# Performance work log

Measured on AMD Instinct MI355X. Metric: run time of the kernel, lower is better.

Reference implementation:

```python
import jax, jax.numpy as jnp
import numpy as np

B, L, H, C, A = 8, 4096, 512, 64, 512
NEG = -1000000000.0

def setup_inputs() -> dict:
    key = jax.random.key(0)
    ks = jax.random.split(key, 6)
    hidden_states = jax.random.normal(ks[0], (B, L, H), dtype=jnp.float32)
    critical_mask = jax.random.randint(ks[1], (B, L, 1), 0, 2).astype(bool)
    count_active_channels = jax.random.randint(ks[2], (B, L, 1), 0, 64).astype(jnp.int32)
    channel_activity = jax.random.normal(ks[3], (B, L, C), dtype=jnp.float32)
    proj_w = jax.random.normal(ks[4], (H, A), dtype=jnp.float32) * 0.02
    proj_b = jnp.zeros((A,), dtype=jnp.float32)
    score_w = jax.random.normal(ks[5], (A, 1), dtype=jnp.float32) * 0.02
    score_b = jnp.zeros((1,), dtype=jnp.float32)
    return {"hidden_states": hidden_states, "critical_mask": critical_mask,
            "count_active_channels": count_active_channels,
            "channel_activity": channel_activity,
            "proj_w": proj_w, "proj_b": proj_b,
            "score_w": score_w, "score_b": score_b}

def reference(hidden_states, critical_mask, count_active_channels, channel_activity,
              proj_w, proj_b, score_w, score_b):
    mask = critical_mask[..., 0].astype(bool)                       # (B,L)
    count_signal = count_active_channels[..., 0].astype(hidden_states.dtype)  # (B,L)
    activity = jnp.maximum(channel_activity.astype(hidden_states.dtype), 0.0)  # (B,L,C)
    # score(tanh(proj(h)))  -> (B,L)
    logits = (jnp.tanh(hidden_states @ proj_w + proj_b) @ score_w + score_b)[..., 0]
    logits = logits + jnp.log1p(jnp.maximum(count_signal, 0.0))
    channel_mask = activity > 0                                      # (B,L,C)
    # (B,C,L) masked logits with log1p activity bias
    channel_logits = logits[:, None, :] + jnp.log1p(jnp.swapaxes(activity, 1, 2))
    channel_logits = jnp.where(jnp.swapaxes(channel_mask, 1, 2), channel_logits, NEG)
    has_channel_any = channel_mask.any(axis=1)                       # (B,C)
    weights = jax.nn.softmax(channel_logits, axis=-1)                # (B,C,L)
    weights = jnp.where(has_channel_any[..., None], weights, 0.0)
    channel_contexts = jnp.einsum('bcl,blh->bch', weights, hidden_states)  # (B,C,H)
    fallback = jnp.broadcast_to(hidden_states[:, -1:, :], channel_contexts.shape)
    channel_contexts = jnp.where(has_channel_any[..., None], channel_contexts, fallback)
    mix = activity / jnp.maximum(activity.sum(axis=2, keepdims=True), 1.0)  # (B,L,C)
    expanded_context = jnp.einsum('blc,bch->blh', mix, channel_contexts)    # (B,L,H)
    max_count = jnp.maximum(count_signal.max(axis=1, keepdims=True), 1.0)
    density_gate = 1.0 + count_signal / max_count                    # (B,L)
    attended = jnp.where(mask[..., None], expanded_context * density_gate[..., None], hidden_states)
    return attended, weights
```

## Files before the change

### kernel.cpp

```cpp
#include <hip/hip_runtime.h>
#include <hip/hip_bf16.h>
#include <math.h>

#define NEGV (-1000000000.0f)
constexpr int Bb = 8, Ll = 4096, Hh = 512, Cc = 64, Aa = 512;

typedef float f32x4 __attribute__((ext_vector_type(4)));
typedef short s16x8 __attribute__((ext_vector_type(8)));

__device__ inline ushort f2bf(float f) {
  union { float f; uint u; } v; v.f = f;
  uint u = v.u;
  return (ushort)((u + 0x7FFFu + ((u >> 16) & 1u)) >> 16);
}

__device__ inline uint bfpack2(float x, float y) {
  __hip_bfloat162 h = __float22bfloat162_rn(make_float2(x, y));
  union { __hip_bfloat162 h; uint u; } v; v.h = h;
  return v.u;
}

__global__ void k_init(const int* __restrict__ cnt, const float* __restrict__ sb,
                       float* __restrict__ logits, int* __restrict__ cmax) {
  int i = blockIdx.x * 256 + threadIdx.x;
  int c = cnt[i];
  logits[i] = sb[0] + log1pf(fmaxf((float)c, 0.f));
  int m = c;
#pragma unroll
  for (int s = 32; s; s >>= 1) m = max(m, __shfl_xor(m, s));
  if ((threadIdx.x & 63) == 0) atomicMax(&cmax[i >> 12], m);
}

__global__ void kT_pw(const float* __restrict__ pw, ushort* __restrict__ pwT) {
  __shared__ ushort s[64][65];
  const int k0 = (blockIdx.x >> 3) * 64, a0 = (blockIdx.x & 7) * 64;
  const int t = threadIdx.x;
#pragma unroll
  for (int i = 0; i < 16; ++i) {
    int e = t + i * 256;
    int kk = e >> 6, aa = e & 63;
    s[aa][kk] = f2bf(pw[(size_t)(k0 + kk) * Aa + a0 + aa]);
  }
  __syncthreads();
#pragma unroll
  for (int i = 0; i < 16; ++i) {
    int e = t + i * 256;
    int aa = e >> 6, kk = e & 63;
    pwT[(size_t)(a0 + aa) * Hh + k0 + kk] = s[aa][kk];
  }
}

__global__ __launch_bounds__(256) void k0_gemm(
    const float* __restrict__ hid, const ushort* __restrict__ pwT,
    const float* __restrict__ pb, const float* __restrict__ sw,
    float* __restrict__ logits) {
  __shared__ ushort At[128 * 40];
  __shared__ ushort Bt[128 * 40];
  const int bm = blockIdx.x, bn = blockIdx.y;
  const int tid = threadIdx.x;
  const int lane = tid & 63;
  const int w = tid >> 6;
  const int wm = w >> 1, wn = w & 1;
  const int lc = lane & 15, lq = lane >> 4;

  const int sr = tid >> 1;
  const int sk = (tid & 1) * 16;

  const float* Ag = hid + ((size_t)(bm * 128 + sr)) * Hh + sk;
  const ushort* Bg = pwT + ((size_t)(bn * 128 + sr)) * Hh + sk;

  f32x4 acc[4][4];
#pragma unroll
  for (int mi = 0; mi < 4; ++mi)
#pragma unroll
    for (int ni = 0; ni < 4; ++ni) acc[mi][ni] = (f32x4){0.f, 0.f, 0.f, 0.f};

  int aoff[4], boff[4];
#pragma unroll
  for (int i = 0; i < 4; ++i) {
    aoff[i] = (wm * 64 + i * 16 + lc) * 40 + lq * 8;
    boff[i] = (wn * 64 + i * 16 + lc) * 40 + lq * 8;
  }

  float4 a0 = *(const float4*)(Ag + 0), a1 = *(const float4*)(Ag + 4),
         a2 = *(const float4*)(Ag + 8), a3 = *(const float4*)(Ag + 12);
  uint4 b0 = *(const uint4*)(Bg + 0), b1 = *(const uint4*)(Bg + 8);

  for (int kb = 0; kb < 16; ++kb) {
    __syncthreads();
    uint4 p0 = {bfpack2(a0.x, a0.y), bfpack2(a0.z, a0.w),
                bfpack2(a1.x, a1.y), bfpack2(a1.z, a1.w)};
    uint4 p1 = {bfpack2(a2.x, a2.y), bfpack2(a2.z, a2.w),
                bfpack2(a3.x, a3.y), bfpack2(a3.z, a3.w)};
    *(uint4*)(At + sr * 40 + sk) = p0;
    *(uint4*)(At + sr * 40 + sk + 8) = p1;
    *(uint4*)(Bt + sr * 40 + sk) = b0;
    *(uint4*)(Bt + sr * 40 + sk + 8) = b1;
    __syncthreads();
    if (kb < 15) {
      const float* ag = Ag + (kb + 1) * 32;
      const ushort* bg = Bg + (kb + 1) * 32;
      a0 = *(const float4*)(ag + 0); a1 = *(const float4*)(ag + 4);
      a2 = *(const float4*)(ag + 8); a3 = *(const float4*)(ag + 12);
      b0 = *(const uint4*)(bg + 0); b1 = *(const uint4*)(bg + 8);
    }
    s16x8 af[4], bf[4];
#pragma unroll
    for (int mi = 0; mi < 4; ++mi) af[mi] = *(const s16x8*)(At + aoff[mi]);
#pragma unroll
    for (int ni = 0; ni < 4; ++ni) bf[ni] = *(const s16x8*)(Bt + boff[ni]);
#pragma unroll
    for (int mi = 0; mi < 4; ++mi)
#pragma unroll
      for (int ni = 0; ni < 4; ++ni)
        acc[mi][ni] = __builtin_amdgcn_mfma_f32_16x16x32_bf16(
            af[mi], bf[ni], acc[mi][ni], 0, 0, 0);
  }

  float pbv[4], swv[4];
#pragma unroll
  for (int ni = 0; ni < 4; ++ni) {
    int n = bn * 128 + wn * 64 + ni * 16 + lc;
    pbv[ni] = pb[n];
    swv[ni] = sw[n];
  }
#pragma unroll
  for (int mi = 0; mi < 4; ++mi) {
#pragma unroll
    for (int r = 0; r < 4; ++r) {
      float s = 0.f;
#pragma unroll
      for (int ni = 0; ni < 4; ++ni) {
        float x = acc[mi][ni][r] + pbv[ni];
        float e = __expf(2.f * x);
        float th = 1.f - 2.f / (e + 1.f);
        s = fmaf(th, swv[ni], s);
      }
      s += __shfl_xor(s, 1);
      s += __shfl_xor(s, 2);
      s += __shfl_xor(s, 4);
      s += __shfl_xor(s, 8);
      if (lc == 0) {
        int m = bm * 128 + wm * 64 + mi * 16 + lq * 4 + r;
        atomicAdd(&logits[m], s);
      }
    }
  }
}

__global__ void k2_transpose(const float* __restrict__ act,
                             float* __restrict__ actT,
                             float* __restrict__ dinv) {
  __shared__ float t64[64][65];
  const int b = blockIdx.x >> 6;
  const int l0 = (blockIdx.x & 63) * 64;
  const int tid = threadIdx.x;
#pragma unroll
  for (int i = 0; i < 16; ++i) {
    int e = tid + i * 256;
    int l = e >> 6, c = e & 63;
    float v = act[((size_t)(b * Ll + l0 + l)) * Cc + c];
    t64[l][c] = fmaxf(v, 0.f);
  }
  __syncthreads();
  if (tid < 64) {
    float s = 0.f;
#pragma unroll 8
    for (int c = 0; c < 64; ++c) s += t64[tid][c];
    dinv[b * Ll + l0 + tid] = 1.0f / fmaxf(s, 1.0f);
  }
#pragma unroll
  for (int i = 0; i < 16; ++i) {
    int e = tid + i * 256;
    int c = e >> 6, lq = e & 63;
    actT[((size_t)(b * Cc + c)) * Ll + l0 + lq] = t64[lq][c];
  }
}

__global__ void k3_softmax(const float* __restrict__ actT,
                           const float* __restrict__ logits,
                           float* __restrict__ wout,
                           ushort* __restrict__ wb16,
                           int* __restrict__ hasany) {
  __shared__ float rmax[4], rcnt[4], rsum[4];
  const int bid = blockIdx.x;
  const int b = bid >> 6;
  const int tid = threadIdx.x;
  const float* arow = actT + (size_t)bid * Ll;

  float xs[16];
  float lmax = NEGV, fcnt = 0.f;
#pragma unroll
  for (int i = 0; i < 16; ++i) {
    int l = tid + i * 256;
    float a = arow[l];
    float x;
    if (a > 0.f) {
      x = logits[b * Ll + l] + log1pf(a);
      fcnt += 1.f;
    } else {
      x = NEGV;
    }
    xs[i] = x;
    lmax = fmaxf(lmax, x);
  }
#pragma unroll
  for (int m = 32; m >= 1; m >>= 1) {
    lmax = fmaxf(lmax, __shfl_xor(lmax, m));
    fcnt += __shfl_xor(fcnt, m);
  }
  if ((tid & 63) == 0) { rmax[tid >> 6] = lmax; rcnt[tid >> 6] = fcnt; }
  __syncthreads();
  float m4 = fmaxf(fmaxf(rmax[0], rmax[1]), fmaxf(rmax[2], rmax[3]));
  float call = rcnt[0] + rcnt[1] + rcnt[2] + rcnt[3];

  float lsum = 0.f;
#pragma unroll
  for (int i = 0; i < 16; ++i) {
    float e = expf(xs[i] - m4);
    xs[i] = e;
    lsum += e;
  }
#pragma unroll
  for (int m = 32; m >= 1; m >>= 1) lsum += __shfl_xor(lsum, m);
  if ((tid & 63) == 0) rsum[tid >> 6] = lsum;
  __syncthreads();
  float s = rsum[0] + rsum[1] + rsum[2] + rsum[3];
  int any = call > 0.5f;
  float inv = any ? 1.0f / s : 0.f;
#pragma unroll
  for (int i = 0; i < 16; ++i) {
    float wv = xs[i] * inv;
    wout[(size_t)bid * Ll + tid + i * 256] = wv;
    wb16[(size_t)bid * Ll + tid + i * 256] = f2bf(wv);
  }
  if (tid == 0) hasany[bid] = any;
}

__global__ __launch_bounds__(256) void k5_mfma(
    const ushort* __restrict__ wb16, const float* __restrict__ hid,
    float* __restrict__ pbuf) {
  const int b = blockIdx.x, nt = blockIdx.y, kz = blockIdx.z;
  const int tid = threadIdx.x;
  const int w = tid >> 6, lane = tid & 63;
  const int lc = lane & 15, lq = lane >> 4;
  const int h0 = nt * 128 + w * 32;

  f32x4 acc[4][2];
#pragma unroll
  for (int mi = 0; mi < 4; ++mi)
#pragma unroll
    for (int ni = 0; ni < 2; ++ni) acc[mi][ni] = (f32x4){0.f, 0.f, 0.f, 0.f};

  const ushort* Abase =
      wb16 + (size_t)b * Cc * Ll + (size_t)lc * Ll + kz * 256 + lq * 8;
  const float* Bbase =
      hid + ((size_t)(b * Ll + kz * 256 + lq * 8)) * Hh + h0 + lc;

  for (int kb = 0; kb < 8; ++kb) {
    s16x8 af[4];
#pragma unroll
    for (int mi = 0; mi < 4; ++mi)
      af[mi] = *(const s16x8*)(Abase + (size_t)mi * 16 * Ll + kb * 32);
    s16x8 bf[2];
#pragma unroll
    for (int ni = 0; ni < 2; ++ni) {
      const float* bp = Bbase + (size_t)kb * 32 * Hh + ni * 16;
      uint u0 = bfpack2(bp[0 * Hh], bp[1 * Hh]);
      uint u1 = bfpack2(bp[2 * Hh], bp[3 * Hh]);
      uint u2 = bfpack2(bp[4 * Hh], bp[5 * Hh]);
      uint u3 = bfpack2(bp[6 * Hh], bp[7 * Hh]);
      union { uint4 u4; s16x8 s; } cv;
      cv.u4 = (uint4){u0, u1, u2, u3};
      bf[ni] = cv.s;
    }
#pragma unroll
    for (int mi = 0; mi < 4; ++mi)
#pragma unroll
      for (int ni = 0; ni < 2; ++ni)
        acc[mi][ni] = __builtin_amdgcn_mfma_f32_16x16x32_bf16(
            af[mi], bf[ni], acc[mi][ni], 0, 0, 0);
  }

  const size_t obase = ((size_t)(kz * Bb + b)) * Cc * Hh;
#pragma unroll
  for (int mi = 0; mi < 4; ++mi)
#pragma unroll
    for (int ni = 0; ni < 2; ++ni)
#pragma unroll
      for (int r = 0; r < 4; ++r)
        pbuf[obase + (size_t)(mi * 16 + lq * 4 + r) * Hh + h0 + ni * 16 + lc] =
            acc[mi][ni][r];
}

__global__ void k6_reduce(const float* __restrict__ pbuf,
                          const int* __restrict__ hasany,
                          const float* __restrict__ hid,
                          float* __restrict__ cctx) {
  int idx = blockIdx.x * 256 + threadIdx.x;
  float s = 0.f;
#pragma unroll
  for (int z = 0; z < 16; ++z) s += pbuf[(size_t)z * 262144 + idx];
  int bc = idx >> 9, b = idx >> 15, h = idx & 511;
  cctx[idx] = hasany[bc] ? s : hid[((size_t)(b * Ll + Ll - 1)) * Hh + h];
}

__global__ __launch_bounds__(256, 2) void k7_out(
    const float* __restrict__ hid, const float* __restrict__ act,
    const float* __restrict__ dinv, const float* __restrict__ cctx,
    const int* __restrict__ mask, const int* __restrict__ cnt,
    const int* __restrict__ cmax, float* __restrict__ out) {
  __shared__ float mix[32 * 68];
  __shared__ float gateb[32];
  __shared__ int maskb[32];
  const int b = blockIdx.x;
  const int l0 = blockIdx.y * 32;
  const int tid = threadIdx.x;
  const float maxcf = fmaxf((float)cmax[b], 1.0f);

#pragma unroll
  for (int i = 0; i < 2; ++i) {
    int q = tid + i * 256;
    int t = q >> 4, cq = q & 15;
    float4 a4 = *(const float4*)(act + ((size_t)(b * Ll + l0 + t)) * Cc + cq * 4);
    float dv = dinv[b * Ll + l0 + t];
    a4.x = fmaxf(a4.x, 0.f) * dv;
    a4.y = fmaxf(a4.y, 0.f) * dv;
    a4.z = fmaxf(a4.z, 0.f) * dv;
    a4.w = fmaxf(a4.w, 0.f) * dv;
    *(float4*)(mix + t * 68 + cq * 4) = a4;
  }
  if (tid < 32) {
    int l = l0 + tid;
    maskb[tid] = mask[b * Ll + l];
    gateb[tid] = 1.0f + (float)cnt[b * Ll + l] / maxcf;
  }
  __syncthreads();

  const int tt = tid >> 6;
  const int h = (tid & 63) * 8;
  float acc[8][8];
#pragma unroll
  for (int t = 0; t < 8; ++t)
#pragma unroll
    for (int u = 0; u < 8; ++u) acc[t][u] = 0.f;

#pragma unroll 4
  for (int c = 0; c < 64; ++c) {
    float4 cA = *(const float4*)(cctx + ((size_t)(b * Cc + c)) * Hh + h);
    float4 cB = *(const float4*)(cctx + ((size_t)(b * Cc + c)) * Hh + h + 4);
    float cv[8] = {cA.x, cA.y, cA.z, cA.w, cB.x, cB.y, cB.z, cB.w};
#pragma unroll
    for (int t = 0; t < 8; ++t) {
      float mv = mix[(tt * 8 + t) * 68 + c];
#pragma unroll
      for (int u = 0; u < 8; ++u) acc[t][u] = fmaf(mv, cv[u], acc[t][u]);
    }
  }
#pragma unroll
  for (int t = 0; t < 8; ++t) {
    int tok = tt * 8 + t;
    size_t off = ((size_t)(b * Ll + l0 + tok)) * Hh + h;
    float4 o1, o2;
    if (maskb[tok]) {
      float g = gateb[tok];
      o1 = make_float4(acc[t][0] * g, acc[t][1] * g, acc[t][2] * g, acc[t][3] * g);
      o2 = make_float4(acc[t][4] * g, acc[t][5] * g, acc[t][6] * g, acc[t][7] * g);
    } else {
      o1 = *(const float4*)(hid + off);
      o2 = *(const float4*)(hid + off + 4);
    }
    *(float4*)(out + off) = o1;
    *(float4*)(out + off + 4) = o2;
  }
}

extern "C" void kernel_launch(void* const* d_in, const int* in_sizes, int n_in,
                              void* d_out, int out_size, void* d_ws,
                              size_t ws_size, hipStream_t stream) {
  const float* hid = (const float*)d_in[0];
  const int* mask = (const int*)d_in[1];
  const int* cnt = (const int*)d_in[2];
  const float* act = (const float*)d_in[3];
  const float* pw = (const float*)d_in[4];
  const float* pb = (const float*)d_in[5];
  const float* sw = (const float*)d_in[6];
  const float* sb = (const float*)d_in[7];

  float* out_att = (float*)d_out;
  float* out_w = out_att + (size_t)Bb * Ll * Hh;

  float* ws = (float*)d_ws;
  float* cctx = ws;
  int* cmaxi = (int*)(ws + 262144);
  float* logits = ws + 262152;
  float* actT = ws + 294920;
  float* dinv = ws + 2392072;
  int* hasany = (int*)(ws + 2424840);
  ushort* pwT = (ushort*)(ws + 2425352);
  ushort* wb16 = (ushort*)(ws + 2556424);
  float* pbuf = ws + 3605000;

  hipMemsetAsync(cmaxi, 0, 8 * sizeof(int), stream);

  k_init<<<128, 256, 0, stream>>>(cnt, sb, logits, cmaxi);
  kT_pw<<<64, 256, 0, stream>>>(pw, pwT);
  k0_gemm<<<dim3(256, 4), 256, 0, stream>>>(hid, pwT, pb, sw, logits);
  k2_transpose<<<512, 256, 0, stream>>>(act, actT, dinv);
  k3_softmax<<<512, 256, 0, stream>>>(actT, logits, out_w, wb16, hasany);
  k5_mfma<<<dim3(8, 4, 16), 256, 0, stream>>>(wb16, hid, pbuf);
  k6_reduce<<<1024, 256, 0, stream>>>(pbuf, hasany, hid, cctx);
  k7_out<<<dim3(8, 128), 256, 0, stream>>>(hid, act, dinv, cctx, mask, cnt,
                                           cmaxi, out_att);
}
```

Baseline: 275.1 us.

## Load GEMM MFMA operands directly from global memory, dropping LDS staging

The projection GEMM no longer stages A and B tiles through shared memory with barriers. Each wave now loads its bf16-packed fragments straight from global memory (L2/cache) and owns a 64x64 output tile, with all four waves in a block sharing the same 64 rows. The grid changes from 256x4 to 512x2 and launch bounds request 4 blocks per CU. This removes LDS traffic and __syncthreads, but it adds redundant global loads with poor coalescing (16-byte strided row reads) and no explicit prefetch.

```diff
diff --git a/kernel.cpp b/kernel.cpp
--- a/kernel.cpp
+++ b/kernel.cpp
@@ -18,6 +18,13 @@
   __hip_bfloat162 h = __float22bfloat162_rn(make_float2(x, y));
   union { __hip_bfloat162 h; uint u; } v; v.h = h;
   return v.u;
+}
+
+__device__ inline s16x8 pack8(const float4 a, const float4 b) {
+  union { uint4 u4; s16x8 s; } cv;
+  cv.u4 = (uint4){bfpack2(a.x, a.y), bfpack2(a.z, a.w),
+                  bfpack2(b.x, b.y), bfpack2(b.z, b.w)};
+  return cv.s;
 }
 
 __global__ void k_init(const int* __restrict__ cnt, const float* __restrict__ sb,
@@ -50,24 +57,15 @@
   }
 }
 
-__global__ __launch_bounds__(256) void k0_gemm(
+__global__ __launch_bounds__(256, 4) void k0_gemm(
     const float* __restrict__ hid, const ushort* __restrict__ pwT,
     const float* __restrict__ pb, const float* __restrict__ sw,
     float* __restrict__ logits) {
-  __shared__ ushort At[128 * 40];
-  __shared__ ushort Bt[128 * 40];
-  const int bm = blockIdx.x, bn = blockIdx.y;
-  const int tid = threadIdx.x;
-  const int lane = tid & 63;
-  const int w = tid >> 6;
-  const int wm = w >> 1, wn = w & 1;
+  const int tid = threadIdx.x;
+  const int w = tid >> 6, lane = tid & 63;
   const int lc = lane & 15, lq = lane >> 4;
-
-  const int sr = tid >> 1;
-  const int sk = (tid & 1) * 16;
-
-  const float* Ag = hid + ((size_t)(bm * 128 + sr)) * Hh + sk;
-  const ushort* Bg = pwT + ((size_t)(bn * 128 + sr)) * Hh + sk;
+  const int m0 = blockIdx.x * 64;
+  const int n0 = (blockIdx.y * 4 + w) * 64;
 
   f32x4 acc[4][4];
 #pragma unroll
@@ -75,40 +73,21 @@
 #pragma unroll
     for (int ni = 0; ni < 4; ++ni) acc[mi][ni] = (f32x4){0.f, 0.f, 0.f, 0.f};
 
-  int aoff[4], boff[4];
-#pragma unroll
-  for (int i = 0; i < 4; ++i) {
-    aoff[i] = (wm * 64 + i * 16 + lc) * 40 + lq * 8;
-    boff[i] = (wn * 64 + i * 16 + lc) * 40 + lq * 8;
-  }
-
-  float4 a0 = *(const float4*)(Ag + 0), a1 = *(const float4*)(Ag + 4),
-         a2 = *(const float4*)(Ag + 8), a3 = *(const float4*)(Ag + 12);
-  uint4 b0 = *(const uint4*)(Bg + 0), b1 = *(const uint4*)(Bg + 8);
+  const float* Abase = hid + ((size_t)(m0 + lc)) * Hh + lq * 8;
+  const ushort* Bbase = pwT + ((size_t)(n0 + lc)) * Hh + lq * 8;
 
   for (int kb = 0; kb < 16; ++kb) {
-    __syncthreads();
-    uint4 p0 = {bfpack2(a0.x, a0.y), bfpack2(a0.z, a0.w),
-                bfpack2(a1.x, a1.y), bfpack2(a1.z, a1.w)};
-    uint4 p1 = {bfpack2(a2.x, a2.y), bfpack2(a2.z, a2.w),
-                bfpack2(a3.x, a3.y), bfpack2(a3.z, a3.w)};
-    *(uint4*)(At + sr * 40 + sk) = p0;
-    *(uint4*)(At + sr * 40 + sk + 8) = p1;
-    *(uint4*)(Bt + sr * 40 + sk) = b0;
-    *(uint4*)(Bt + sr * 40 + sk + 8) = b1;
-    __syncthreads();
-    if (kb < 15) {
-      const float* ag = Ag + (kb + 1) * 32;
-      const ushort* bg = Bg + (kb + 1) * 32;
-      a0 = *(const float4*)(ag + 0); a1 = *(const float4*)(ag + 4);
-      a2 = *(const float4*)(ag + 8); a3 = *(const float4*)(ag + 12);
-      b0 = *(const uint4*)(bg + 0); b1 = *(const uint4*)(bg + 8);
-    }
     s16x8 af[4], bf[4];
 #pragma unroll
-    for (int mi = 0; mi < 4; ++mi) af[mi] = *(const s16x8*)(At + aoff[mi]);
-#pragma unroll
-    for (int ni = 0; ni < 4; ++ni) bf[ni] = *(const s16x8*)(Bt + boff[ni]);
+    for (int mi = 0; mi < 4; ++mi) {
+      const float* ap = Abase + (size_t)mi * 16 * Hh + kb * 32;
+      float4 a0 = *(const float4*)(ap);
+      float4 a1 = *(const float4*)(ap + 4);
+      af[mi] = pack8(a0, a1);
+    }
+#pragma unroll
+    for (int ni = 0; ni < 4; ++ni)
+      bf[ni] = *(const s16x8*)(Bbase + (size_t)ni * 16 * Hh + kb * 32);
 #pragma unroll
     for (int mi = 0; mi < 4; ++mi)
 #pragma unroll
@@ -120,7 +99,7 @@
   float pbv[4], swv[4];
 #pragma unroll
   for (int ni = 0; ni < 4; ++ni) {
-    int n = bn * 128 + wn * 64 + ni * 16 + lc;
+    int n = n0 + ni * 16 + lc;
     pbv[ni] = pb[n];
     swv[ni] = sw[n];
   }
@@ -141,7 +120,7 @@
       s += __shfl_xor(s, 4);
       s += __shfl_xor(s, 8);
       if (lc == 0) {
-        int m = bm * 128 + wm * 64 + mi * 16 + lq * 4 + r;
+        int m = m0 + mi * 16 + lq * 4 + r;
         atomicAdd(&logits[m], s);
       }
     }
@@ -405,7 +384,7 @@
 
   k_init<<<128, 256, 0, stream>>>(cnt, sb, logits, cmaxi);
   kT_pw<<<64, 256, 0, stream>>>(pw, pwT);
-  k0_gemm<<<dim3(256, 4), 256, 0, stream>>>(hid, pwT, pb, sw, logits);
+  k0_gemm<<<dim3(512, 2), 256, 0, stream>>>(hid, pwT, pb, sw, logits);
   k2_transpose<<<512, 256, 0, stream>>>(act, actT, dinv);
   k3_softmax<<<512, 256, 0, stream>>>(actT, logits, out_w, wb16, hasany);
   k5_mfma<<<dim3(8, 4, 16), 256, 0, stream>>>(wb16, hid, pbuf);
```

Result: slower. 313.9 us (+14.1%).
